# Kernel optimization log

Hardware: AMD Instinct MI355X
Metric: run time of the kernel (lower is better)

The kernel has to match this reference:

```python
import jax, jax.numpy as jnp
import numpy as np

H, W = 2048, 2048
K = 32   # number of predicted instance labels (torch.unique(pred_instance_mask))
N = 16   # number of target instance labels (torch.unique(target_mask))
SMOOTH = 1.0
LOG_CLAMP = -100.0  # torch BCELoss clamps log terms at -100


def bce_dice(p, t):
    # BCEDiceLoss = BCELoss(p, t) + (1 - dice(p, t)), torch-style log clamping
    logp = jnp.clip(jnp.log(p), LOG_CLAMP)
    log1p = jnp.clip(jnp.log1p(-p), LOG_CLAMP)
    bce = -jnp.mean(t * logp + (1.0 - t) * log1p)
    inter = jnp.sum(p * t)
    dice = 1.0 - (2.0 * inter + SMOOTH) / (jnp.sum(p) + jnp.sum(t) + SMOOTH)
    return bce + dice


def setup_inputs() -> dict:
    key = jax.random.key(0)
    k1, k2, k3, k4 = jax.random.split(key, 4)
    return {
        "pred_instance_mask": jax.random.randint(k1, (H, W), 0, K, dtype=jnp.int32),
        "pred_score": jax.random.normal(k2, (H, W), dtype=jnp.float32),
        "cls_out": jax.random.uniform(k3, (H, W), dtype=jnp.float32, minval=1e-4, maxval=1.0 - 1e-4),
        "target_mask": jax.random.randint(k4, (H, W), 0, N, dtype=jnp.int32),
    }


def reference(pred_instance_mask, pred_score, cls_out, target_mask):
    hw = float(H * W)
    # MSE(pred_score, zeros)
    res = jnp.mean(pred_score * pred_score)
    # BCEDice(cls_out, (target_mask > 0).float())
    res = res + bce_dice(cls_out, (target_mask > 0).astype(jnp.float32))

    # Batched pairwise BCEDice between binary label masks.
    # Every label in [0,K)/[0,N) is present w.h.p., matching torch.unique output.
    pred_oh = (pred_instance_mask[None] == jnp.arange(K, dtype=jnp.int32)[:, None, None]).astype(jnp.float32)  # [K,H,W]
    tgt_oh = (target_mask[None] == jnp.arange(N, dtype=jnp.int32)[:, None, None]).astype(jnp.float32)          # [N,H,W]

    inter = jnp.einsum("nhw,khw->nk", tgt_oh, pred_oh)  # [N,K]
    sp = jnp.sum(pred_oh, axis=(1, 2))                   # [K]
    st = jnp.sum(tgt_oh, axis=(1, 2))                    # [N]
    union_sum = st[:, None] + sp[None, :]                # [N,K]

    # For binary p,t: elementwise BCE with log-clamp at -100 is 100 where p!=t, 0 where p==t.
    bce = (-LOG_CLAMP) * (union_sum - 2.0 * inter) / hw
    dice = 1.0 - (2.0 * inter + SMOOTH) / (union_sum + SMOOTH)
    pair = bce + dice                                    # [N,K]

    res = res + jnp.sum(jnp.min(pair, axis=1))
    return res / float(N)
```

## Files before the change

kernel.cpp:

```cpp
#include <hip/hip_runtime.h>

#define HW_TOT (2048 * 2048)
#define KLAB 32
#define NLAB 16
#define NBIN (NLAB * KLAB)
#define NREP 32
#define NBLK 1024

typedef int   vint4   __attribute__((ext_vector_type(4)));
typedef float vfloat4 __attribute__((ext_vector_type(4)));


__global__ __launch_bounds__(256) void connect_k1(
    const vint4* __restrict__ pim, const vfloat4* __restrict__ ps,
    const vfloat4* __restrict__ co, const vint4* __restrict__ tm,
    float4* __restrict__ parts, unsigned int* __restrict__ hist2, int nvec)
{
    __shared__ unsigned int lh[NBIN];
    __shared__ float red[4][4];

    for (int i = threadIdx.x; i < NBIN; i += 256) lh[i] = 0u;
    __syncthreads();

    float s2 = 0.f, sp = 0.f, spt = 0.f, sbce = 0.f;

    const int stride = gridDim.x * blockDim.x;
    for (int i = blockIdx.x * blockDim.x + threadIdx.x; i < nvec; i += stride) {
        vint4   pv = __builtin_nontemporal_load(&pim[i]);
        vfloat4 sv = __builtin_nontemporal_load(&ps[i]);
        vfloat4 cv = __builtin_nontemporal_load(&co[i]);
        vint4   tv = __builtin_nontemporal_load(&tm[i]);

#pragma unroll
        for (int j = 0; j < 4; ++j) {
            float s = sv[j];
            float p = cv[j];
            int   t = tv[j];
            int   k = pv[j];

            s2 += s * s;
            sp += p;
            bool tb = (t > 0);
            float sel = tb ? p : (1.0f - p);
            float lg = fmaxf(__logf(sel), -100.0f);
            sbce += lg;
            if (tb) spt += p;

            atomicAdd(&lh[t * KLAB + k], 1u);
        }
    }

#pragma unroll
    for (int off = 32; off > 0; off >>= 1) {
        s2   += __shfl_down(s2, off);
        sp   += __shfl_down(sp, off);
        spt  += __shfl_down(spt, off);
        sbce += __shfl_down(sbce, off);
    }
    int wave = threadIdx.x >> 6;
    if ((threadIdx.x & 63) == 0) {
        red[wave][0] = s2; red[wave][1] = sp; red[wave][2] = spt; red[wave][3] = sbce;
    }
    __syncthreads();

    if (threadIdx.x == 0) {
        float4 r;
        r.x = red[0][0] + red[1][0] + red[2][0] + red[3][0];
        r.y = red[0][1] + red[1][1] + red[2][1] + red[3][1];
        r.z = red[0][2] + red[1][2] + red[2][2] + red[3][2];
        r.w = red[0][3] + red[1][3] + red[2][3] + red[3][3];
        parts[blockIdx.x] = r;
    }

    unsigned int* rep = hist2 + (blockIdx.x & (NREP - 1)) * NBIN;
    for (int i = threadIdx.x; i < NBIN; i += 256) {
        unsigned int v = lh[i];
        if (v) atomicAdd(&rep[i], v);
    }
}

__global__ __launch_bounds__(512) void connect_fin(
    const unsigned int* __restrict__ hist2, const float4* __restrict__ parts,
    int B, float* __restrict__ out)
{
    __shared__ float  fh[NBIN];
    __shared__ double sred[8][4];
    __shared__ float  rowmin[NLAB];
    __shared__ float  strow[NLAB];

    int tid = threadIdx.x;

    unsigned int h = 0u;
#pragma unroll
    for (int c = 0; c < NREP; ++c) h += hist2[c * NBIN + tid];
    fh[tid] = (float)h;

    double s2 = 0.0, sp = 0.0, spt = 0.0, sbce = 0.0;
    for (int b = tid; b < B; b += 512) {
        float4 r = parts[b];
        s2 += r.x; sp += r.y; spt += r.z; sbce += r.w;
    }
#pragma unroll
    for (int off = 32; off > 0; off >>= 1) {
        s2   += __shfl_down(s2, off);
        sp   += __shfl_down(sp, off);
        spt  += __shfl_down(spt, off);
        sbce += __shfl_down(sbce, off);
    }
    if ((tid & 63) == 0) {
        int w = tid >> 6;
        sred[w][0] = s2; sred[w][1] = sp; sred[w][2] = spt; sred[w][3] = sbce;
    }
    __syncthreads();

    int n = tid >> 5;
    int k = tid & 31;

    float st = 0.f, spk = 0.f;
#pragma unroll
    for (int kk = 0; kk < KLAB; ++kk) st += fh[n * KLAB + kk];
#pragma unroll
    for (int nn = 0; nn < NLAB; ++nn) spk += fh[nn * KLAB + k];

    float I   = fh[n * KLAB + k];
    float uni = st + spk;
    float pair = 100.0f * (uni - 2.0f * I) / (float)HW_TOT
               + 1.0f - (2.0f * I + 1.0f) / (uni + 1.0f);

    float v = pair;
#pragma unroll
    for (int off = 16; off > 0; off >>= 1) v = fminf(v, __shfl_xor(v, off));

    if (k == 0) { rowmin[n] = v; strow[n] = st; }
    __syncthreads();

    if (tid == 0) {
        double S2 = 0, SP = 0, SPT = 0, SBCE = 0;
#pragma unroll
        for (int w = 0; w < 8; ++w) {
            S2 += sred[w][0]; SP += sred[w][1]; SPT += sred[w][2]; SBCE += sred[w][3];
        }
        double hw = (double)HW_TOT;
        double res = S2 / hw;
        res += -SBCE / hw;
        double sum_t = hw - (double)strow[0];
        res += 1.0 - (2.0 * SPT + 1.0) / (SP + sum_t + 1.0);
        float pm = 0.f;
#pragma unroll
        for (int i = 0; i < NLAB; ++i) pm += rowmin[i];
        res += (double)pm;
        out[0] = (float)(res / (double)NLAB);
    }
}

extern "C" void kernel_launch(void* const* d_in, const int* in_sizes, int n_in,
                              void* d_out, int out_size, void* d_ws, size_t ws_size,
                              hipStream_t stream) {
    const vint4*   pim = (const vint4*)d_in[0];
    const vfloat4* ps  = (const vfloat4*)d_in[1];
    const vfloat4* co  = (const vfloat4*)d_in[2];
    const vint4*   tm  = (const vint4*)d_in[3];
    float* out = (float*)d_out;

    unsigned int* hist2 = (unsigned int*)d_ws;
    float4*       parts = (float4*)((char*)d_ws + (size_t)NREP * NBIN * 4);

    (void)hipMemsetAsync(hist2, 0, (size_t)NREP * NBIN * 4, stream);

    const int nvec = HW_TOT / 4;
    connect_k1<<<NBLK, 256, 0, stream>>>(pim, ps, co, tm, parts, hist2, nvec);
    connect_fin<<<1, 512, 0, stream>>>(hist2, parts, NBLK, out);
}
```

Baseline: 23.66 us.

## Fuse finalize kernel into main kernel via last-block ticket

```diff
diff --git a/kernel.cpp b/kernel.cpp
--- a/kernel.cpp
+++ b/kernel.cpp
@@ -11,13 +11,15 @@
 typedef float vfloat4 __attribute__((ext_vector_type(4)));
 
 
-__global__ __launch_bounds__(256) void connect_k1(
+__global__ __launch_bounds__(256) void connect_fused(
     const vint4* __restrict__ pim, const vfloat4* __restrict__ ps,
     const vfloat4* __restrict__ co, const vint4* __restrict__ tm,
-    float4* __restrict__ parts, unsigned int* __restrict__ hist2, int nvec)
+    float4* __restrict__ parts, unsigned int* __restrict__ hist2,
+    unsigned int* __restrict__ ticket, float* __restrict__ out, int nvec)
 {
     __shared__ unsigned int lh[NBIN];
     __shared__ float red[4][4];
+    __shared__ int   isLast;
 
     for (int i = threadIdx.x; i < NBIN; i += 256) lh[i] = 0u;
     __syncthreads();
@@ -32,11 +34,11 @@
         vint4   tv = __builtin_nontemporal_load(&tm[i]);
 
 #pragma unroll
-        for (int j = 0; j < 4; ++j) {
-            float s = sv[j];
-            float p = cv[j];
-            int   t = tv[j];
-            int   k = pv[j];
+        for (int e = 0; e < 4; ++e) {
+            float s = sv[e];
+            float p = cv[e];
+            int   t = tv[e];
+            int   k = pv[e];
 
             s2 += s * s;
             sp += p;
@@ -77,67 +79,87 @@
         unsigned int v = lh[i];
         if (v) atomicAdd(&rep[i], v);
     }
-}
 
-__global__ __launch_bounds__(512) void connect_fin(
-    const unsigned int* __restrict__ hist2, const float4* __restrict__ parts,
-    int B, float* __restrict__ out)
-{
+    __syncthreads();
+    if (threadIdx.x == 0) {
+        __threadfence();
+        unsigned int t = atomicAdd(ticket, 1u);
+        isLast = (t == NBLK - 1);
+    }
+    __syncthreads();
+    if (!isLast) return;
+    __threadfence();
+
     __shared__ float  fh[NBIN];
-    __shared__ double sred[8][4];
+    __shared__ double sred[4][4];
     __shared__ float  rowmin[NLAB];
     __shared__ float  strow[NLAB];
 
     int tid = threadIdx.x;
 
-    unsigned int h = 0u;
+    unsigned int h0 = 0u, h1 = 0u;
 #pragma unroll
-    for (int c = 0; c < NREP; ++c) h += hist2[c * NBIN + tid];
-    fh[tid] = (float)h;
+    for (int c = 0; c < NREP; ++c) {
+        h0 += hist2[c * NBIN + tid];
+        h1 += hist2[c * NBIN + tid + 256];
+    }
+    fh[tid]       = (float)h0;
+    fh[tid + 256] = (float)h1;
 
-    double s2 = 0.0, sp = 0.0, spt = 0.0, sbce = 0.0;
-    for (int b = tid; b < B; b += 512) {
-        float4 r = parts[b];
-        s2 += r.x; sp += r.y; spt += r.z; sbce += r.w;
+    double d2 = 0.0, dp = 0.0, dpt = 0.0, dbce = 0.0;
+#pragma unroll
+    for (int b = 0; b < NBLK / 256; ++b) {
+        float4 r = parts[tid + b * 256];
+        d2 += r.x; dp += r.y; dpt += r.z; dbce += r.w;
     }
 #pragma unroll
     for (int off = 32; off > 0; off >>= 1) {
-        s2   += __shfl_down(s2, off);
-        sp   += __shfl_down(sp, off);
-        spt  += __shfl_down(spt, off);
-        sbce += __shfl_down(sbce, off);
+        d2   += __shfl_down(d2, off);
+        dp   += __shfl_down(dp, off);
+        dpt  += __shfl_down(dpt, off);
+        dbce += __shfl_down(dbce, off);
     }
     if ((tid & 63) == 0) {
         int w = tid >> 6;
-        sred[w][0] = s2; sred[w][1] = sp; sred[w][2] = spt; sred[w][3] = sbce;
+        sred[w][0] = d2; sred[w][1] = dp; sred[w][2] = dpt; sred[w][3] = dbce;
     }
     __syncthreads();
 
-    int n = tid >> 5;
-    int k = tid & 31;
+    int n0 = tid >> 5;
+    int n1 = n0 + 8;
+    int k  = tid & 31;
 
-    float st = 0.f, spk = 0.f;
+    float st0 = 0.f, st1 = 0.f, spk = 0.f;
 #pragma unroll
-    for (int kk = 0; kk < KLAB; ++kk) st += fh[n * KLAB + kk];
+    for (int kk = 0; kk < KLAB; ++kk) {
+        st0 += fh[n0 * KLAB + kk];
+        st1 += fh[n1 * KLAB + kk];
+    }
 #pragma unroll
     for (int nn = 0; nn < NLAB; ++nn) spk += fh[nn * KLAB + k];
 
-    float I   = fh[n * KLAB + k];
-    float uni = st + spk;
-    float pair = 100.0f * (uni - 2.0f * I) / (float)HW_TOT
-               + 1.0f - (2.0f * I + 1.0f) / (uni + 1.0f);
+    float I0 = fh[n0 * KLAB + k], I1 = fh[n1 * KLAB + k];
+    float u0 = st0 + spk,         u1 = st1 + spk;
+    float pair0 = 100.0f * (u0 - 2.0f * I0) / (float)HW_TOT
+                + 1.0f - (2.0f * I0 + 1.0f) / (u0 + 1.0f);
+    float pair1 = 100.0f * (u1 - 2.0f * I1) / (float)HW_TOT
+                + 1.0f - (2.0f * I1 + 1.0f) / (u1 + 1.0f);
 
-    float v = pair;
 #pragma unroll
-    for (int off = 16; off > 0; off >>= 1) v = fminf(v, __shfl_xor(v, off));
-
-    if (k == 0) { rowmin[n] = v; strow[n] = st; }
+    for (int off = 16; off > 0; off >>= 1) {
+        pair0 = fminf(pair0, __shfl_xor(pair0, off));
+        pair1 = fminf(pair1, __shfl_xor(pair1, off));
+    }
+    if (k == 0) {
+        rowmin[n0] = pair0; strow[n0] = st0;
+        rowmin[n1] = pair1; strow[n1] = st1;
+    }
     __syncthreads();
 
     if (tid == 0) {
         double S2 = 0, SP = 0, SPT = 0, SBCE = 0;
 #pragma unroll
-        for (int w = 0; w < 8; ++w) {
+        for (int w = 0; w < 4; ++w) {
             S2 += sred[w][0]; SP += sred[w][1]; SPT += sred[w][2]; SBCE += sred[w][3];
         }
         double hw = (double)HW_TOT;
@@ -162,12 +184,12 @@
     const vint4*   tm  = (const vint4*)d_in[3];
     float* out = (float*)d_out;
 
-    unsigned int* hist2 = (unsigned int*)d_ws;
-    float4*       parts = (float4*)((char*)d_ws + (size_t)NREP * NBIN * 4);
+    unsigned int* hist2  = (unsigned int*)d_ws;
+    unsigned int* ticket = hist2 + NREP * NBIN;
+    float4*       parts  = (float4*)((char*)d_ws + (size_t)NREP * NBIN * 4 + 16);
 
-    (void)hipMemsetAsync(hist2, 0, (size_t)NREP * NBIN * 4, stream);
+    (void)hipMemsetAsync(hist2, 0, (size_t)NREP * NBIN * 4 + 16, stream);
 
     const int nvec = HW_TOT / 4;
-    connect_k1<<<NBLK, 256, 0, stream>>>(pim, ps, co, tm, parts, hist2, nvec);
-    connect_fin<<<1, 512, 0, stream>>>(hist2, parts, NBLK, out);
+    connect_fused<<<NBLK, 256, 0, stream>>>(pim, ps, co, tm, parts, hist2, ticket, out, nvec);
 }
```

Result: slower. 51.62 us (+118.2%).

## Replace global histogram atomics and memset with packed per-block partial histograms

Applied to the files above, without the earlier changes.

```diff
diff --git a/kernel.cpp b/kernel.cpp
--- a/kernel.cpp
+++ b/kernel.cpp
@@ -4,22 +4,22 @@
 #define KLAB 32
 #define NLAB 16
 #define NBIN (NLAB * KLAB)
-#define NREP 32
-#define NBLK 1024
+#define NBLK 512
+#define BTHR 512
 
 typedef int   vint4   __attribute__((ext_vector_type(4)));
 typedef float vfloat4 __attribute__((ext_vector_type(4)));
 
 
-__global__ __launch_bounds__(256) void connect_k1(
+__global__ __launch_bounds__(BTHR) void connect_k1(
     const vint4* __restrict__ pim, const vfloat4* __restrict__ ps,
     const vfloat4* __restrict__ co, const vint4* __restrict__ tm,
-    float4* __restrict__ parts, unsigned int* __restrict__ hist2, int nvec)
+    float4* __restrict__ parts, unsigned int* __restrict__ hist1, int nvec)
 {
     __shared__ unsigned int lh[NBIN];
-    __shared__ float red[4][4];
+    __shared__ float red[8][4];
 
-    for (int i = threadIdx.x; i < NBIN; i += 256) lh[i] = 0u;
+    lh[threadIdx.x] = 0u;
     __syncthreads();
 
     float s2 = 0.f, sp = 0.f, spt = 0.f, sbce = 0.f;
@@ -32,11 +32,11 @@
         vint4   tv = __builtin_nontemporal_load(&tm[i]);
 
 #pragma unroll
-        for (int j = 0; j < 4; ++j) {
-            float s = sv[j];
-            float p = cv[j];
-            int   t = tv[j];
-            int   k = pv[j];
+        for (int e = 0; e < 4; ++e) {
+            float s = sv[e];
+            float p = cv[e];
+            int   t = tv[e];
+            int   k = pv[e];
 
             s2 += s * s;
             sp += p;
@@ -64,53 +64,65 @@
     __syncthreads();
 
     if (threadIdx.x == 0) {
-        float4 r;
-        r.x = red[0][0] + red[1][0] + red[2][0] + red[3][0];
-        r.y = red[0][1] + red[1][1] + red[2][1] + red[3][1];
-        r.z = red[0][2] + red[1][2] + red[2][2] + red[3][2];
-        r.w = red[0][3] + red[1][3] + red[2][3] + red[3][3];
+        float4 r = {0.f, 0.f, 0.f, 0.f};
+#pragma unroll
+        for (int w = 0; w < 8; ++w) {
+            r.x += red[w][0]; r.y += red[w][1]; r.z += red[w][2]; r.w += red[w][3];
+        }
         parts[blockIdx.x] = r;
     }
 
-    unsigned int* rep = hist2 + (blockIdx.x & (NREP - 1)) * NBIN;
-    for (int i = threadIdx.x; i < NBIN; i += 256) {
-        unsigned int v = lh[i];
-        if (v) atomicAdd(&rep[i], v);
+    if (threadIdx.x < NBIN / 2) {
+        unsigned int w = lh[2 * threadIdx.x] | (lh[2 * threadIdx.x + 1] << 16);
+        hist1[blockIdx.x * (NBIN / 2) + threadIdx.x] = w;
     }
 }
 
 __global__ __launch_bounds__(512) void connect_fin(
-    const unsigned int* __restrict__ hist2, const float4* __restrict__ parts,
-    int B, float* __restrict__ out)
+    const unsigned int* __restrict__ hist1, const float4* __restrict__ parts,
+    float* __restrict__ out)
 {
     __shared__ float  fh[NBIN];
+    __shared__ unsigned int ph[2][NBIN];
     __shared__ double sred[8][4];
     __shared__ float  rowmin[NLAB];
     __shared__ float  strow[NLAB];
 
     int tid = threadIdx.x;
 
-    unsigned int h = 0u;
-#pragma unroll
-    for (int c = 0; c < NREP; ++c) h += hist2[c * NBIN + tid];
-    fh[tid] = (float)h;
+    {
+        int col  = tid & 255;
+        int half = tid >> 8;
+        unsigned int s0 = 0u, s1 = 0u;
+#pragma unroll 8
+        for (int b = half * 256; b < half * 256 + 256; ++b) {
+            unsigned int w = hist1[b * (NBIN / 2) + col];
+            s0 += w & 0xFFFFu;
+            s1 += w >> 16;
+        }
+        ph[half][2 * col]     = s0;
+        ph[half][2 * col + 1] = s1;
+    }
 
-    double s2 = 0.0, sp = 0.0, spt = 0.0, sbce = 0.0;
-    for (int b = tid; b < B; b += 512) {
-        float4 r = parts[b];
-        s2 += r.x; sp += r.y; spt += r.z; sbce += r.w;
+    double d2, dp, dpt, dbce;
+    {
+        float4 r = parts[tid];
+        d2 = r.x; dp = r.y; dpt = r.z; dbce = r.w;
     }
 #pragma unroll
     for (int off = 32; off > 0; off >>= 1) {
-        s2   += __shfl_down(s2, off);
-        sp   += __shfl_down(sp, off);
-        spt  += __shfl_down(spt, off);
-        sbce += __shfl_down(sbce, off);
+        d2   += __shfl_down(d2, off);
+        dp   += __shfl_down(dp, off);
+        dpt  += __shfl_down(dpt, off);
+        dbce += __shfl_down(dbce, off);
     }
     if ((tid & 63) == 0) {
         int w = tid >> 6;
-        sred[w][0] = s2; sred[w][1] = sp; sred[w][2] = spt; sred[w][3] = sbce;
+        sred[w][0] = d2; sred[w][1] = dp; sred[w][2] = dpt; sred[w][3] = dbce;
     }
+    __syncthreads();
+
+    fh[tid] = (float)(ph[0][tid] + ph[1][tid]);
     __syncthreads();
 
     int n = tid >> 5;
@@ -162,12 +174,10 @@
     const vint4*   tm  = (const vint4*)d_in[3];
     float* out = (float*)d_out;
 
-    unsigned int* hist2 = (unsigned int*)d_ws;
-    float4*       parts = (float4*)((char*)d_ws + (size_t)NREP * NBIN * 4);
-
-    (void)hipMemsetAsync(hist2, 0, (size_t)NREP * NBIN * 4, stream);
+    unsigned int* hist1 = (unsigned int*)d_ws;
+    float4*       parts = (float4*)((char*)d_ws + (size_t)NBLK * (NBIN / 2) * 4);
 
     const int nvec = HW_TOT / 4;
-    connect_k1<<<NBLK, 256, 0, stream>>>(pim, ps, co, tm, parts, hist2, nvec);
-    connect_fin<<<1, 512, 0, stream>>>(hist2, parts, NBLK, out);
+    connect_k1<<<NBLK, BTHR, 0, stream>>>(pim, ps, co, tm, parts, hist1, nvec);
+    connect_fin<<<1, 512, 0, stream>>>(hist1, parts, out);
 }
```

New measurement: 25.35 us. 7.1% more time.
